# Performance work log

Hardware: AMD Instinct MI355X
Metric: run time of the kernel (lower is better)

Reference implementation:

```python
import jax, jax.numpy as jnp
import numpy as np

NEG_SLOPE = 0.2  # PyG GATConv default leaky_relu slope


def gat_conv(x, src, dst, W, att_src, att_dst, bias, num_nodes):
    """PyG-style GATConv with concat=False (mean over heads).
    x: [N, Fin], src/dst: [E] (self-loops already appended),
    W: [Fin, H*C], att_src/att_dst: [H, C], bias: [C].
    """
    H, C = att_src.shape
    h = (x @ W).reshape(num_nodes, H, C)               # [N, H, C]
    a_s = jnp.sum(h * att_src[None], axis=-1)          # [N, H]
    a_d = jnp.sum(h * att_dst[None], axis=-1)          # [N, H]
    e = jax.nn.leaky_relu(a_s[src] + a_d[dst], NEG_SLOPE)  # [E, H]
    # softmax over incoming edges per destination node
    e_max = jax.ops.segment_max(e, dst, num_segments=num_nodes)  # [N, H]
    e_exp = jnp.exp(e - e_max[dst])
    denom = jax.ops.segment_sum(e_exp, dst, num_segments=num_nodes)
    alpha = e_exp / (denom[dst] + 1e-16)               # [E, H]
    msg = h[src] * alpha[:, :, None]                   # [E, H, C]
    out = jax.ops.segment_sum(msg, dst, num_segments=num_nodes)  # [N, H, C]
    return out.mean(axis=1) + bias                     # concat=False -> head mean


def setup_inputs() -> dict:
    N, E = 100000, 1600000
    Fin, Hid, Fout, Hds = 128, 64, 32, 2
    key = jax.random.key(0)
    ks = jax.random.split(key, 12)
    glorot = lambda k, shape, fan: (jax.random.normal(k, shape, jnp.float32) / np.sqrt(fan))
    return {
        "x": jax.random.normal(ks[0], (N, Fin), jnp.float32),
        "edge_index": jax.random.randint(ks[1], (2, E), 0, N, jnp.int64 if jax.config.read("jax_enable_x64") else jnp.int32),
        "W1": glorot(ks[2], (Fin, Hds * Hid), Fin),
        "att_src1": glorot(ks[3], (Hds, Hid), Hid),
        "att_dst1": glorot(ks[4], (Hds, Hid), Hid),
        "b1": jnp.zeros((Hid,), jnp.float32),
        "W2": glorot(ks[5], (Hid, Hds * Fout), Hid),
        "att_src2": glorot(ks[6], (Hds, Fout), Fout),
        "att_dst2": glorot(ks[7], (Hds, Fout), Fout),
        "b2": jnp.zeros((Fout,), jnp.float32),
    }


def reference(x, edge_index, W1, att_src1, att_dst1, b1, W2, att_src2, att_dst2, b2):
    N = x.shape[0]
    # PyG GATConv default: add self-loops
    loops = jnp.arange(N, dtype=edge_index.dtype)
    src = jnp.concatenate([edge_index[0], loops])
    dst = jnp.concatenate([edge_index[1], loops])
    # dropout(p=0.6) is identity in eval mode
    h = gat_conv(x, src, dst, W1, att_src1, att_dst1, b1, N)
    h = jax.nn.elu(h)
    out = gat_conv(h, src, dst, W2, att_src2, att_dst2, b2, N)
    return out
```

## Files before the change

kernel.cpp:

```cpp
#include <hip/hip_runtime.h>
#include <hip/hip_bf16.h>
#include <hip/hip_fp16.h>
#include <math.h>


#define BINBITS 9
#define NBUCK 256
#define CHUNK 2048
#define SPANCAP 12288

typedef _Float16 half8 __attribute__((ext_vector_type(8)));
typedef float f32x4 __attribute__((ext_vector_type(4)));


__global__ void bucket_hist_kernel(const int* __restrict__ dst, int* __restrict__ bcnt, int E,
                                   const float* __restrict__ W1, _Float16* __restrict__ Wt1,
                                   const float* __restrict__ W2, _Float16* __restrict__ Wt2) {
    __shared__ int h[NBUCK];
    int t = threadIdx.x;
    h[t] = 0;
    __syncthreads();
    for (int i = blockIdx.x * blockDim.x + t; i < E; i += gridDim.x * blockDim.x)
        atomicAdd(&h[dst[i] >> BINBITS], 1);
    for (int i = blockIdx.x * blockDim.x + t; i < 128 * 128 + 64 * 64;
         i += gridDim.x * blockDim.x) {
        if (i < 128 * 128) {
            int nn = i >> 7, k = i & 127;
            Wt1[i] = (_Float16)W1[k * 128 + nn];
        } else {
            int j = i - 128 * 128;
            int nn = j >> 6, k = j & 63;
            Wt2[j] = (_Float16)W2[k * 64 + nn];
        }
    }
    __syncthreads();
    if (h[t]) atomicAdd(&bcnt[t], h[t]);
}

__launch_bounds__(256)
__global__ void binA_kernel(const int* __restrict__ esrc, const int* __restrict__ edst,
                            const int* __restrict__ bcnt, int* __restrict__ bfill,
                            unsigned* __restrict__ binned, int E) {
    __shared__ unsigned stage[CHUNK];
    __shared__ int hcnt[NBUCK], hexc[NBUCK], gb[NBUCK], hfill[NBUCK], gbase[NBUCK];
    const int tid = threadIdx.x;
    const int c0 = blockIdx.x * CHUNK;
    const int n = min(CHUNK, E - c0);

    hcnt[tid] = 0;
    hfill[tid] = 0;
    int myg = bcnt[tid];
    gbase[tid] = myg;
    __syncthreads();
    for (int i = tid; i < n; i += 256) atomicAdd(&hcnt[edst[c0 + i] >> BINBITS], 1);
    __syncthreads();
    int myc = hcnt[tid];
    hexc[tid] = myc;
    __syncthreads();
    for (int o = 1; o < NBUCK; o <<= 1) {
        int x = (tid >= o) ? hexc[tid - o] : 0;
        int y = (tid >= o) ? gbase[tid - o] : 0;
        __syncthreads();
        hexc[tid] += x;
        gbase[tid] += y;
        __syncthreads();
    }
    hexc[tid] -= myc;
    int gexc = gbase[tid] - myg;
    gb[tid] = myc ? (gexc + atomicAdd(&bfill[tid], myc)) : 0;
    __syncthreads();

    for (int i = tid; i < n; i += 256) {
        int d = edst[c0 + i], s = esrc[c0 + i];
        int b = d >> BINBITS;
        int p = hexc[b] + atomicAdd(&hfill[b], 1);
        stage[p] = ((unsigned)(d & ((1 << BINBITS) - 1)) << 17) | (unsigned)s;
    }
    __syncthreads();

    const int wid = tid >> 6, lane = tid & 63;
    const int sg = lane >> 4, sl = lane & 15;
    for (int bb = wid * 64; bb < wid * 64 + 64; bb += 4) {
        int b = bb + sg;
        int cnt = hcnt[b], sb = hexc[b], g = gb[b];
        for (int l = sl; l < cnt; l += 16) binned[g + l] = stage[sb + l];
    }
}

__launch_bounds__(512)
__global__ void binB_kernel(const unsigned* __restrict__ binned, const int* __restrict__ bcnt,
                            int* __restrict__ rowptr, int* __restrict__ csr, int N) {
    __shared__ int cnt[512];
    __shared__ int sscan[512];
    __shared__ int excl[513];
    __shared__ int stag[SPANCAP];
    __shared__ int sE0, sE1;
    const int tid = threadIdx.x;
    const int b = blockIdx.x;
    const int node0 = b << BINBITS;
    if (node0 >= N) return;
    const int nn = min(512, N - node0);

    if (tid < NBUCK) sscan[tid] = bcnt[tid];
    cnt[tid] = (tid < nn) ? 1 : 0;
    __syncthreads();
    for (int o = 1; o < NBUCK; o <<= 1) {
        int x = (tid < NBUCK && tid >= o) ? sscan[tid - o] : 0;
        __syncthreads();
        if (tid < NBUCK) sscan[tid] += x;
        __syncthreads();
    }
    if (tid == b) {
        sE1 = sscan[b];
        sE0 = sscan[b] - bcnt[b];
    }
    __syncthreads();
    const int e0 = sE0, e1 = sE1;

    for (int i = e0 + tid; i < e1; i += 512)
        atomicAdd(&cnt[binned[i] >> 17], 1);
    __syncthreads();

    int v = cnt[tid];
    sscan[tid] = v;
    __syncthreads();
    for (int o = 1; o < 512; o <<= 1) {
        int x = (tid >= o) ? sscan[tid - o] : 0;
        __syncthreads();
        sscan[tid] += x;
        __syncthreads();
    }
    excl[tid] = sscan[tid] - v;
    if (tid == 511) excl[512] = sscan[511];
    __syncthreads();

    const int rbase = e0 + node0;
    if (tid < nn) rowptr[node0 + tid] = rbase + excl[tid];
    if (node0 + nn >= N && tid == 0) rowptr[N] = rbase + excl[512];

    cnt[tid] = 0;
    __syncthreads();
    const int span = excl[512];

    if (span <= SPANCAP) {
        for (int i = e0 + tid; i < e1; i += 512) {
            unsigned e = binned[i];
            int dloc = e >> 17, src = e & 0x1FFFF;
            int p = excl[dloc] + atomicAdd(&cnt[dloc], 1);
            stag[p] = src;
        }
        if (tid < nn) {
            int p = excl[tid] + atomicAdd(&cnt[tid], 1);
            stag[p] = node0 + tid;
        }
        __syncthreads();
        for (int i = tid; i < span; i += 512) csr[rbase + i] = stag[i];
    } else {
        for (int i = e0 + tid; i < e1; i += 512) {
            unsigned e = binned[i];
            int dloc = e >> 17, src = e & 0x1FFFF;
            csr[rbase + excl[dloc] + atomicAdd(&cnt[dloc], 1)] = src;
        }
        if (tid < nn)
            csr[rbase + excl[tid] + atomicAdd(&cnt[tid], 1)] = node0 + tid;
    }
}


template <int FIN, int FOUT, typename XT>
__launch_bounds__(256)
__global__ void gemm_attn_mfma(const XT* __restrict__ X, const _Float16* __restrict__ Wt,
                               const float* __restrict__ atts, const float* __restrict__ attd,
                               __half* __restrict__ Hh, float* __restrict__ a_s,
                               float* __restrict__ a_d, int N) {
    constexpr int BM = 128;
    constexpr int C = FOUT / 2;
    constexpr int NT = FOUT / 16;
    constexpr int KS = FIN / 32;
    constexpr int HT = C / 16;
    __shared__ _Float16 sA[BM * FIN];
    __shared__ _Float16 sB[FOUT * FIN];

    const int tid = threadIdx.x;
    const int wv = tid >> 6, ln = tid & 63;
    const int lm = ln & 15, quad = ln >> 4;
    const int row0 = blockIdx.x * BM;

    if (sizeof(XT) == 4) {
        for (int idx = tid; idx < BM * FIN / 4; idx += 256) {
            int r = idx / (FIN / 4), c4 = idx % (FIN / 4);
            int gr = row0 + r;
            float4 v = make_float4(0.f, 0.f, 0.f, 0.f);
            if (gr < N) v = *(const float4*)&((const float*)X)[(size_t)gr * FIN + c4 * 4];
            _Float16 h4[4] = {(_Float16)v.x, (_Float16)v.y, (_Float16)v.z, (_Float16)v.w};
            *(float2*)&sA[r * FIN + c4 * 4] = *(float2*)h4;
        }
    } else {
        for (int idx = tid; idx < BM * FIN / 8; idx += 256) {
            int r = idx / (FIN / 8), c8 = idx % (FIN / 8);
            int gr = row0 + r;
            int4 v = make_int4(0, 0, 0, 0);
            if (gr < N) v = *(const int4*)&((const __half*)X)[(size_t)gr * FIN + c8 * 8];
            *(int4*)&sA[r * FIN + c8 * 8] = v;
        }
    }
    for (int idx = tid; idx < FOUT * FIN / 8; idx += 256)
        *(int4*)&sB[idx * 8] = *(const int4*)&Wt[idx * 8];
    __syncthreads();

    f32x4 acc[2][NT];
#pragma unroll
    for (int mt = 0; mt < 2; ++mt)
#pragma unroll
        for (int nt = 0; nt < NT; ++nt) acc[mt][nt] = f32x4{0.f, 0.f, 0.f, 0.f};

    const int r0 = wv * 32 + lm;
#pragma unroll
    for (int ks = 0; ks < KS; ++ks) {
        int k0 = ks * 32 + quad * 8;
        half8 a0 = *(const half8*)&sA[r0 * FIN + k0];
        half8 a1 = *(const half8*)&sA[(r0 + 16) * FIN + k0];
#pragma unroll
        for (int nt = 0; nt < NT; ++nt) {
            half8 b = *(const half8*)&sB[(nt * 16 + lm) * FIN + k0];
            acc[0][nt] = __builtin_amdgcn_mfma_f32_16x16x32_f16(a0, b, acc[0][nt], 0, 0, 0);
            acc[1][nt] = __builtin_amdgcn_mfma_f32_16x16x32_f16(a1, b, acc[1][nt], 0, 0, 0);
        }
    }

    float psum[2][4][2], pdum[2][4][2];
#pragma unroll
    for (int mt = 0; mt < 2; ++mt)
#pragma unroll
        for (int r = 0; r < 4; ++r) {
            psum[mt][r][0] = psum[mt][r][1] = 0.f;
            pdum[mt][r][0] = pdum[mt][r][1] = 0.f;
        }
#pragma unroll
    for (int nt = 0; nt < NT; ++nt) {
        float av = atts[nt * 16 + lm];
        float dv = attd[nt * 16 + lm];
        int hh = nt / HT;
#pragma unroll
        for (int mt = 0; mt < 2; ++mt)
#pragma unroll
            for (int r = 0; r < 4; ++r) {
                psum[mt][r][hh] = fmaf(acc[mt][nt][r], av, psum[mt][r][hh]);
                pdum[mt][r][hh] = fmaf(acc[mt][nt][r], dv, pdum[mt][r][hh]);
            }
    }
#pragma unroll
    for (int o = 1; o < 16; o <<= 1) {
#pragma unroll
        for (int mt = 0; mt < 2; ++mt)
#pragma unroll
            for (int r = 0; r < 4; ++r) {
                psum[mt][r][0] += __shfl_xor(psum[mt][r][0], o);
                psum[mt][r][1] += __shfl_xor(psum[mt][r][1], o);
                pdum[mt][r][0] += __shfl_xor(pdum[mt][r][0], o);
                pdum[mt][r][1] += __shfl_xor(pdum[mt][r][1], o);
            }
    }
    if (lm == 0) {
#pragma unroll
        for (int mt = 0; mt < 2; ++mt)
#pragma unroll
            for (int r = 0; r < 4; ++r) {
                int gr = row0 + wv * 32 + mt * 16 + quad * 4 + r;
                if (gr < N) {
                    *(float2*)&a_s[gr * 2] = make_float2(psum[mt][r][0], psum[mt][r][1]);
                    *(float2*)&a_d[gr * 2] = make_float2(pdum[mt][r][0], pdum[mt][r][1]);
                }
            }
    }

    __syncthreads();
    _Float16* sH = sA;
#pragma unroll
    for (int mt = 0; mt < 2; ++mt)
#pragma unroll
        for (int nt = 0; nt < NT; ++nt)
#pragma unroll
            for (int r = 0; r < 4; ++r)
                sH[(wv * 32 + mt * 16 + quad * 4 + r) * FOUT + nt * 16 + lm] =
                    (_Float16)acc[mt][nt][r];
    __syncthreads();
    for (int idx = tid; idx < BM * FOUT / 8; idx += 256) {
        int r = idx / (FOUT / 8), c8 = idx % (FOUT / 8);
        int gr = row0 + r;
        if (gr < N)
            *(int4*)&Hh[(size_t)gr * FOUT + c8 * 8] = *(const int4*)&sH[r * FOUT + c8 * 8];
    }
}


__device__ __forceinline__ float lrelu02(float x) { return x > 0.f ? x : 0.2f * x; }

template <int C, bool ELU, typename OT>
__launch_bounds__(256)
__global__ void aggregate_kernel(const __half* __restrict__ Hh,
                                 const float* __restrict__ a_s, const float* __restrict__ a_d,
                                 const int* __restrict__ rowptr, const int* __restrict__ csr,
                                 const float* __restrict__ bias, OT* __restrict__ out, int N) {
    constexpr int LPE = (C == 64) ? 16 : 8;
    constexpr int NG = 64 / LPE;
    constexpr int RI = C / 4;
    const int wid = threadIdx.x >> 6;
    const int lane = threadIdx.x & 63;
    const int sub = lane & (LPE - 1);
    const int qid = lane / LPE;
    const int myH = (sub >= LPE / 2);
    int n = blockIdx.x * 4 + wid;
    if (n >= N) return;
    int start = rowptr[n], end = rowptr[n + 1];
    const int4* HI = (const int4*)Hh;
    float2 adn = ((const float2*)a_d)[n];

    float av[8];
#pragma unroll
    for (int j = 0; j < 8; ++j) av[j] = 0.f;
    float d0 = 0.f, d1 = 0.f;

    for (int cs = start; cs < end; cs += 64) {
        int j = cs + lane;
        int s = 0;
        if (j < end) s = csr[j];
        int sri = (int)((unsigned)s * RI);
        int cnt = min(64, end - cs);
        int nbatch = (cnt + NG - 1) / NG;

        float2 asv = ((const float2*)a_s)[s];
        float e0 = 0.f, e1 = 0.f;
        if (j < end) {
            e0 = __expf(lrelu02(asv.x + adn.x));
            e1 = __expf(lrelu02(asv.y + adn.y));
        }
        d0 += e0;
        d1 += e1;

        int b = 0;
        for (; b + 4 <= nbatch; b += 4) {
            int adr[4];
#pragma unroll
            for (int u = 0; u < 4; ++u)
                adr[u] = __shfl(sri, (b + u) * NG + qid);
            int4 hv[4];
#pragma unroll
            for (int u = 0; u < 4; ++u)
                hv[u] = HI[(unsigned)adr[u] + (unsigned)sub];
#pragma unroll
            for (int u = 0; u < 4; ++u) {
                int slot = (b + u) * NG + qid;
                float w0 = __shfl(e0, slot);
                float w1 = __shfl(e1, slot);
                float ww = myH ? w1 : w0;
                const _Float16* hh = (const _Float16*)&hv[u];
#pragma unroll
                for (int k = 0; k < 8; ++k)
                    av[k] = fmaf(ww, (float)hh[k], av[k]);
            }
        }
        if constexpr (C == 32) {
            int rem = nbatch - b;
            if (rem > 0) {
                int4 hvr[3];
#pragma unroll
                for (int u = 0; u < 3; ++u) {
                    if (u < rem) {
                        int adr = __shfl(sri, (b + u) * NG + qid);
                        hvr[u] = HI[(unsigned)adr + (unsigned)sub];
                    }
                }
#pragma unroll
                for (int u = 0; u < 3; ++u) {
                    if (u < rem) {
                        int slot = (b + u) * NG + qid;
                        float w0 = __shfl(e0, slot);
                        float w1 = __shfl(e1, slot);
                        float ww = myH ? w1 : w0;
                        const _Float16* hh = (const _Float16*)&hvr[u];
#pragma unroll
                        for (int k = 0; k < 8; ++k)
                            av[k] = fmaf(ww, (float)hh[k], av[k]);
                    }
                }
            }
        } else {
            for (; b < nbatch; ++b) {
                int slot = b * NG + qid;
                int adr = __shfl(sri, slot);
                int4 hv = HI[(unsigned)adr + (unsigned)sub];
                float w0 = __shfl(e0, slot);
                float w1 = __shfl(e1, slot);
                float ww = myH ? w1 : w0;
                const _Float16* hh = (const _Float16*)&hv;
#pragma unroll
                for (int k = 0; k < 8; ++k)
                    av[k] = fmaf(ww, (float)hh[k], av[k]);
            }
        }
    }

#pragma unroll
    for (int o = LPE; o < 64; o <<= 1)
#pragma unroll
        for (int j = 0; j < 8; ++j) av[j] += __shfl_xor(av[j], o);
#pragma unroll
    for (int o = 32; o > 0; o >>= 1) {
        d0 += __shfl_xor(d0, o);
        d1 += __shfl_xor(d1, o);
    }
    float sc = myH ? (0.5f / d1) : (0.5f / d0);
#pragma unroll
    for (int j = 0; j < 8; ++j) av[j] *= sc;
#pragma unroll
    for (int j = 0; j < 8; ++j) av[j] += __shfl_xor(av[j], LPE / 2);

    if (lane < LPE / 2) {
        float4 b0 = *(const float4*)(bias + sub * 8);
        float4 b1 = *(const float4*)(bias + sub * 8 + 4);
        float o0[8];
        o0[0] = av[0] + b0.x; o0[1] = av[1] + b0.y;
        o0[2] = av[2] + b0.z; o0[3] = av[3] + b0.w;
        o0[4] = av[4] + b1.x; o0[5] = av[5] + b1.y;
        o0[6] = av[6] + b1.z; o0[7] = av[7] + b1.w;
        if (ELU) {
#pragma unroll
            for (int j = 0; j < 8; ++j) o0[j] = o0[j] > 0.f ? o0[j] : expm1f(o0[j]);
        }
        if (sizeof(OT) == 2) {
            union { int4 v; __half2 h2[4]; } u;
#pragma unroll
            for (int p = 0; p < 4; ++p) u.h2[p] = __floats2half2_rn(o0[2 * p], o0[2 * p + 1]);
            *(int4*)((__half*)out + (size_t)n * C + sub * 8) = u.v;
        } else {
            *(float4*)((float*)out + (size_t)n * C + sub * 8) =
                make_float4(o0[0], o0[1], o0[2], o0[3]);
            *(float4*)((float*)out + (size_t)n * C + sub * 8 + 4) =
                make_float4(o0[4], o0[5], o0[6], o0[7]);
        }
    }
}


extern "C" void kernel_launch(void* const* d_in, const int* in_sizes, int n_in,
                              void* d_out, int out_size, void* d_ws, size_t ws_size,
                              hipStream_t stream) {
    const float* x    = (const float*)d_in[0];
    const int*   eidx = (const int*)d_in[1];
    const float* W1   = (const float*)d_in[2];
    const float* as1w = (const float*)d_in[3];
    const float* ad1w = (const float*)d_in[4];
    const float* b1   = (const float*)d_in[5];
    const float* W2   = (const float*)d_in[6];
    const float* as2w = (const float*)d_in[7];
    const float* ad2w = (const float*)d_in[8];
    const float* b2   = (const float*)d_in[9];
    float* out = (float*)d_out;

    const int N = in_sizes[0] / 128;
    const int E = in_sizes[1] / 2;
    const int NBK = (N + (1 << BINBITS) - 1) >> BINBITS;

    char* base = (char*)d_ws;
    size_t off = 0;
    auto alloc = [&](size_t bytes) {
        size_t cur = off;
        off += (bytes + 255) & ~(size_t)255;
        return (void*)(base + cur);
    };

    int* rowptr   = (int*)alloc((size_t)(N + 1) * 4);
    int* csr      = (int*)alloc((size_t)(E + N) * 4);
    int* bcbf     = (int*)alloc((size_t)512 * 4);
    unsigned* binned = (unsigned*)alloc((size_t)E * 4);
    __half* h1    = (__half*)alloc((size_t)N * 128 * 2);
    __half* x2h   = (__half*)alloc((size_t)N * 64 * 2);
    float* a_s    = (float*)alloc((size_t)N * 2 * 4);
    float* a_d    = (float*)alloc((size_t)N * 2 * 4);
    _Float16* Wt1 = (_Float16*)alloc((size_t)128 * 128 * 2);
    _Float16* Wt2 = (_Float16*)alloc((size_t)64 * 64 * 2);

    int* bcnt  = bcbf;
    int* bfill = bcbf + 256;
    const int* esrc = eidx;
    const int* edst = eidx + E;

    hipMemsetAsync(bcbf, 0, 512 * 4, stream);
    bucket_hist_kernel<<<256, 256, 0, stream>>>(edst, bcnt, E, W1, Wt1, W2, Wt2);
    binA_kernel<<<(E + CHUNK - 1) / CHUNK, 256, 0, stream>>>(esrc, edst, bcnt, bfill, binned, E);
    binB_kernel<<<NBK, 512, 0, stream>>>(binned, bcnt, rowptr, csr, N);

    gemm_attn_mfma<128, 128, float>
        <<<(N + 127) / 128, 256, 0, stream>>>(x, Wt1, as1w, ad1w, h1, a_s, a_d, N);
    aggregate_kernel<64, true, __half>
        <<<(N + 3) / 4, 256, 0, stream>>>(h1, a_s, a_d, rowptr, csr, b1, x2h, N);

    gemm_attn_mfma<64, 64, __half>
        <<<(N + 127) / 128, 256, 0, stream>>>(x2h, Wt2, as2w, ad2w, h1, a_s, a_d, N);
    aggregate_kernel<32, false, float>
        <<<(N + 3) / 4, 256, 0, stream>>>(h1, a_s, a_d, rowptr, csr, b2, out, N);
}
```

Baseline: 333.9 us.

## Fuse bucket histogram into first GEMM launch and transpose weights in-kernel

Removes the separate histogram/weight-transpose kernel. The first 256 blocks of the layer-1 GEMM launch now compute the destination-bucket histogram, and every GEMM block builds its fp16 transposed weight tile directly from the fp32 weights. This saves one launch and overlaps the histogram with the GEMM. In exchange, every GEMM block re-reads and converts the weights with strided loads, and the GEMM now runs before the binning kernels instead of after them.

```diff
diff --git a/kernel.cpp b/kernel.cpp
--- a/kernel.cpp
+++ b/kernel.cpp
@@ -12,30 +12,6 @@
 typedef _Float16 half8 __attribute__((ext_vector_type(8)));
 typedef float f32x4 __attribute__((ext_vector_type(4)));
 
-
-__global__ void bucket_hist_kernel(const int* __restrict__ dst, int* __restrict__ bcnt, int E,
-                                   const float* __restrict__ W1, _Float16* __restrict__ Wt1,
-                                   const float* __restrict__ W2, _Float16* __restrict__ Wt2) {
-    __shared__ int h[NBUCK];
-    int t = threadIdx.x;
-    h[t] = 0;
-    __syncthreads();
-    for (int i = blockIdx.x * blockDim.x + t; i < E; i += gridDim.x * blockDim.x)
-        atomicAdd(&h[dst[i] >> BINBITS], 1);
-    for (int i = blockIdx.x * blockDim.x + t; i < 128 * 128 + 64 * 64;
-         i += gridDim.x * blockDim.x) {
-        if (i < 128 * 128) {
-            int nn = i >> 7, k = i & 127;
-            Wt1[i] = (_Float16)W1[k * 128 + nn];
-        } else {
-            int j = i - 128 * 128;
-            int nn = j >> 6, k = j & 63;
-            Wt2[j] = (_Float16)W2[k * 64 + nn];
-        }
-    }
-    __syncthreads();
-    if (h[t]) atomicAdd(&bcnt[t], h[t]);
-}
 
 __launch_bounds__(256)
 __global__ void binA_kernel(const int* __restrict__ esrc, const int* __restrict__ edst,
@@ -169,10 +145,12 @@
 
 template <int FIN, int FOUT, typename XT>
 __launch_bounds__(256)
-__global__ void gemm_attn_mfma(const XT* __restrict__ X, const _Float16* __restrict__ Wt,
+__global__ void gemm_attn_mfma(const XT* __restrict__ X, const float* __restrict__ W,
                                const float* __restrict__ atts, const float* __restrict__ attd,
                                __half* __restrict__ Hh, float* __restrict__ a_s,
-                               float* __restrict__ a_d, int N) {
+                               float* __restrict__ a_d, int N,
+                               const int* __restrict__ edst, int* __restrict__ bcnt, int E,
+                               int histBlocks) {
     constexpr int BM = 128;
     constexpr int C = FOUT / 2;
     constexpr int NT = FOUT / 16;
@@ -182,9 +160,21 @@
     __shared__ _Float16 sB[FOUT * FIN];
 
     const int tid = threadIdx.x;
+
+    if (blockIdx.x < histBlocks) {
+        int* h = (int*)sA;
+        h[tid] = 0;
+        __syncthreads();
+        for (int i = blockIdx.x * 256 + tid; i < E; i += histBlocks * 256)
+            atomicAdd(&h[edst[i] >> BINBITS], 1);
+        __syncthreads();
+        if (h[tid]) atomicAdd(&bcnt[tid], h[tid]);
+        return;
+    }
+
     const int wv = tid >> 6, ln = tid & 63;
     const int lm = ln & 15, quad = ln >> 4;
-    const int row0 = blockIdx.x * BM;
+    const int row0 = (blockIdx.x - histBlocks) * BM;
 
     if (sizeof(XT) == 4) {
         for (int idx = tid; idx < BM * FIN / 4; idx += 256) {
@@ -204,8 +194,14 @@
             *(int4*)&sA[r * FIN + c8 * 8] = v;
         }
     }
-    for (int idx = tid; idx < FOUT * FIN / 8; idx += 256)
-        *(int4*)&sB[idx * 8] = *(const int4*)&Wt[idx * 8];
+    for (int idx = tid; idx < FOUT * FIN / 8; idx += 256) {
+        int n = idx / (FIN / 8);
+        int k8 = (idx % (FIN / 8)) * 8;
+        _Float16 t8[8];
+#pragma unroll
+        for (int j = 0; j < 8; ++j) t8[j] = (_Float16)W[(size_t)(k8 + j) * FOUT + n];
+        *(int4*)&sB[n * FIN + k8] = *(const int4*)t8;
+    }
     __syncthreads();
 
     f32x4 acc[2][NT];
@@ -478,8 +474,6 @@
     __half* x2h   = (__half*)alloc((size_t)N * 64 * 2);
     float* a_s    = (float*)alloc((size_t)N * 2 * 4);
     float* a_d    = (float*)alloc((size_t)N * 2 * 4);
-    _Float16* Wt1 = (_Float16*)alloc((size_t)128 * 128 * 2);
-    _Float16* Wt2 = (_Float16*)alloc((size_t)64 * 64 * 2);
 
     int* bcnt  = bcbf;
     int* bfill = bcbf + 256;
@@ -487,17 +481,21 @@
     const int* edst = eidx + E;
 
     hipMemsetAsync(bcbf, 0, 512 * 4, stream);
-    bucket_hist_kernel<<<256, 256, 0, stream>>>(edst, bcnt, E, W1, Wt1, W2, Wt2);
+
+    const int gemm1Blocks = (N + 127) / 128;
+    gemm_attn_mfma<128, 128, float>
+        <<<256 + gemm1Blocks, 256, 0, stream>>>(x, W1, as1w, ad1w, h1, a_s, a_d, N,
+                                                edst, bcnt, E, 256);
+
     binA_kernel<<<(E + CHUNK - 1) / CHUNK, 256, 0, stream>>>(esrc, edst, bcnt, bfill, binned, E);
     binB_kernel<<<NBK, 512, 0, stream>>>(binned, bcnt, rowptr, csr, N);
 
-    gemm_attn_mfma<128, 128, float>
-        <<<(N + 127) / 128, 256, 0, stream>>>(x, Wt1, as1w, ad1w, h1, a_s, a_d, N);
     aggregate_kernel<64, true, __half>
         <<<(N + 3) / 4, 256, 0, stream>>>(h1, a_s, a_d, rowptr, csr, b1, x2h, N);
 
     gemm_attn_mfma<64, 64, __half>
-        <<<(N + 127) / 128, 256, 0, stream>>>(x2h, Wt2, as2w, ad2w, h1, a_s, a_d, N);
+        <<<(N + 127) / 128, 256, 0, stream>>>(x2h, W2, as2w, ad2w, h1, a_s, a_d, N,
+                                              nullptr, nullptr, 0, 0);
     aggregate_kernel<32, false, float>
         <<<(N + 3) / 4, 256, 0, stream>>>(h1, a_s, a_d, rowptr, csr, b2, out, N);
 }
```

After: 341.6 us. +2.3%, slower.
